# Optimization experiments

Measured on AMD Instinct MI355X. Metric: run time of the kernel, lower is better.

Reference implementation:

```python
import jax, jax.numpy as jnp
from jax import lax
import numpy as np

EPS = 1e-5


def ref_points(Hk, Wk):
    # torch linspace(0.5, Hk-0.5, Hk)/Hk * 2 - 1, stacked (y, x)
    ys = (jnp.linspace(0.5, Hk - 0.5, Hk) / Hk) * 2.0 - 1.0
    xs = (jnp.linspace(0.5, Wk - 0.5, Wk) / Wk) * 2.0 - 1.0
    yy, xx = jnp.meshgrid(ys, xs, indexing='ij')
    return jnp.stack([yy, xx], axis=-1)  # (Hk, Wk, 2) in (y, x) order


def grid_sample(img, grid):
    # Bilinear, align_corners=True, zeros padding (torch F.grid_sample defaults).
    # img: (N, C, Hi, Wi); grid: (N, Hg, Wg, 2) with (x, y) in [-1, 1].
    N, C, Hi, Wi = img.shape
    Hg, Wg = grid.shape[1], grid.shape[2]
    gx = (grid[..., 0] + 1.0) * 0.5 * (Wi - 1)
    gy = (grid[..., 1] + 1.0) * 0.5 * (Hi - 1)
    x0 = jnp.floor(gx)
    y0 = jnp.floor(gy)
    wx1 = gx - x0
    wy1 = gy - y0
    imgf = img.reshape(N, C, Hi * Wi)

    def corner(ix, iy, w):
        valid = (ix >= 0) & (ix < Wi) & (iy >= 0) & (iy < Hi)
        idx = (jnp.clip(iy, 0, Hi - 1).astype(jnp.int32) * Wi
               + jnp.clip(ix, 0, Wi - 1).astype(jnp.int32)).reshape(N, -1)
        vals = jax.vmap(lambda im, f: im[:, f])(imgf, idx)  # (N, C, Hg*Wg)
        return vals * (w * valid).reshape(N, 1, -1)

    out = (corner(x0, y0, (1 - wx1) * (1 - wy1))
           + corner(x0 + 1, y0, wx1 * (1 - wy1))
           + corner(x0, y0 + 1, (1 - wx1) * wy1)
           + corner(x0 + 1, y0 + 1, wx1 * wy1))
    return out.reshape(N, C, Hg, Wg)


def setup_inputs() -> dict:
    key = jax.random.key(0)
    ks = jax.random.split(key, 8)
    B, C, H, W = 8, 128, 64, 64
    gc, nH = 64, 4
    return {
        'x': jax.random.normal(ks[0], (B, C, H, W), jnp.float32),
        'w_dw': jax.random.normal(ks[1], (gc, 1, 5, 5), jnp.float32) * 0.1,
        'ln_w': jnp.ones((gc,), jnp.float32),
        'w_off': jax.random.normal(ks[2], (3, gc), jnp.float32) * 0.1,
        'wq': jax.random.normal(ks[3], (C, C), jnp.float32) * 0.05,
        'wk': jax.random.normal(ks[4], (C, C), jnp.float32) * 0.05,
        'wv': jax.random.normal(ks[5], (C, C), jnp.float32) * 0.05,
        'wo': jax.random.normal(ks[6], (C, C), jnp.float32) * 0.05,
        'rpe': jax.random.normal(ks[7], (nH, 2 * H - 1, 2 * W - 1), jnp.float32) * 0.01,
    }


def reference(x, w_dw, ln_w, w_off, wq, wk, wv, wo, rpe):
    B, C, H, W = x.shape
    G, nH = 2, 4
    gc = C // G           # group channels
    dh = C // nH          # head channels
    gh = nH // G          # heads per group
    scale = dh ** -0.5
    orf = 1.0             # offset_range_factor

    conv1x1 = lambda t, w: jnp.einsum('oi,bihw->bohw', w, t)

    q = conv1x1(x, wq)                                    # (B, C, H, W)
    q_off = q.reshape(B * G, gc, H, W)

    # conv_offset: depthwise 5x5 stride 4 pad 2 -> BiasFree LN (over C) -> GELU -> 1x1 to 3
    off = lax.conv_general_dilated(q_off, w_dw, (4, 4), ((2, 2), (2, 2)),
                                   dimension_numbers=('NCHW', 'OIHW', 'NCHW'),
                                   feature_group_count=gc)  # (B*G, gc, Hk, Wk)
    var = jnp.var(off, axis=1, keepdims=True)
    off = off / jnp.sqrt(var + EPS) * ln_w.reshape(1, -1, 1, 1)
    off = jax.nn.gelu(off, approximate=False)
    off = jnp.einsum('oi,bihw->bohw', w_off, off)          # (B*G, 3, Hk, Wk)

    Hk, Wk = off.shape[2], off.shape[3]
    n = Hk * Wk

    # channel 0 = y offset, channel 1 = x offset, channel 2 = modulation
    offset = jnp.stack([jnp.tanh(off[:, 0]) * (orf / Hk),
                        jnp.tanh(off[:, 1]) * (orf / Wk)], axis=-1)  # (B*G, Hk, Wk, 2) (y,x)
    dm = jax.nn.sigmoid(off[:, 2])[:, None]                # (B*G, 1, Hk, Wk)

    pos = offset + ref_points(Hk, Wk)[None]                # (B*G, Hk, Wk, 2) (y,x)

    xs = grid_sample(x.reshape(B * G, gc, H, W), pos[..., ::-1])  # grid in (x,y)
    xs = (xs * dm).reshape(B, C, 1, n)

    k = conv1x1(xs, wk).reshape(B * nH, dh, n)
    v = conv1x1(xs, wv).reshape(B * nH, dh, n)
    qf = q.reshape(B * nH, dh, H * W)

    attn = jnp.einsum('bcm,bcn->bmn', qf, k) * scale       # (B*nH, H*W, n)

    # relative-position bias sampled at continuous displacements
    rpe_b = jnp.broadcast_to(rpe[None], (B, nH, 2 * H - 1, 2 * W - 1)
                             ).reshape(B * G, gh, 2 * H - 1, 2 * W - 1)
    qg = ref_points(H, W).reshape(H * W, 2)                # (H*W, 2)
    disp = (qg[None, :, None, :] - pos.reshape(B * G, 1, n, 2)) * 0.5  # (B*G, H*W, n, 2)
    bias = grid_sample(rpe_b, disp[..., ::-1]).reshape(B * nH, H * W, n)

    attn = jax.nn.softmax(attn + bias, axis=2)
    out = jnp.einsum('bmn,bcn->bcm', attn, v).reshape(B, C, H, W)
    return conv1x1(out, wo)
```

## Files before the change

kernel.cpp:

```cpp
#include <hip/hip_runtime.h>
#include <hip/hip_bf16.h>
#include <math.h>

#define HW 4096
#define NCH 128

typedef __attribute__((ext_vector_type(8))) short short8;
typedef __attribute__((ext_vector_type(4))) float f32x4;

__device__ __forceinline__ short f2bf(float f) {
  union { __hip_bfloat16 h; short s; } u;
  u.h = __float2bfloat16(f);
  return u.s;
}
__device__ __forceinline__ float bf2f(short s) {
  union { unsigned u; float f; } u;
  u.u = ((unsigned)(unsigned short)s) << 16;
  return u.f;
}

__global__ __launch_bounds__(256) void xq_kernel(
    const float* __restrict__ x, const float* __restrict__ wq,
    short* __restrict__ xT, float* __restrict__ qT) {
  __shared__ float s[128][65];
  int tid = threadIdx.x;
  int b = blockIdx.y;
  int m0 = blockIdx.x * 64;
  {
    int ml = tid & 63, ch = tid >> 6;
#pragma unroll
    for (int i = 0; i < 32; ++i) {
      int c = i * 4 + ch;
      s[c][ml] = x[((size_t)(b * NCH + c)) * HW + m0 + ml];
    }
  }
  __syncthreads();
  {
    int c = tid & 127, mh = tid >> 7;
#pragma unroll
    for (int i = 0; i < 32; ++i) {
      int m = i * 2 + mh;
      xT[((size_t)(b * HW + m0 + m)) * NCH + c] = f2bf(s[c][m]);
    }
  }
  int w = tid >> 6, lane = tid & 63, l15 = lane & 15, qd = lane >> 4;
  int mrow = w * 16 + l15;
  f32x4 acc[8];
#pragma unroll
  for (int ot = 0; ot < 8; ++ot) acc[ot] = (f32x4){0.f, 0.f, 0.f, 0.f};
#pragma unroll
  for (int kc = 0; kc < 4; ++kc) {
    short8 ah, al;
#pragma unroll
    for (int j = 0; j < 8; ++j) {
      float v = s[kc * 32 + qd * 8 + j][mrow];
      short hi = f2bf(v);
      ah[j] = hi;
      al[j] = f2bf(v - bf2f(hi));
    }
#pragma unroll
    for (int ot = 0; ot < 8; ++ot) {
      const float* wr = wq + (size_t)(ot * 16 + l15) * NCH + kc * 32 + qd * 8;
      f32x4 w0 = *(const f32x4*)wr;
      f32x4 w1 = *(const f32x4*)(wr + 4);
      short8 bh, bl;
#pragma unroll
      for (int j = 0; j < 4; ++j) {
        short h0 = f2bf(w0[j]);
        bh[j] = h0;
        bl[j] = f2bf(w0[j] - bf2f(h0));
        short h1 = f2bf(w1[j]);
        bh[4 + j] = h1;
        bl[4 + j] = f2bf(w1[j] - bf2f(h1));
      }
      acc[ot] = __builtin_amdgcn_mfma_f32_16x16x32_bf16(ah, bh, acc[ot], 0, 0, 0);
      acc[ot] = __builtin_amdgcn_mfma_f32_16x16x32_bf16(al, bh, acc[ot], 0, 0, 0);
      acc[ot] = __builtin_amdgcn_mfma_f32_16x16x32_bf16(ah, bl, acc[ot], 0, 0, 0);
    }
  }
#pragma unroll
  for (int ot = 0; ot < 8; ++ot)
#pragma unroll
    for (int r = 0; r < 4; ++r)
      qT[((size_t)(b * HW + m0 + w * 16 + qd * 4 + r)) * NCH + ot * 16 + l15] =
          acc[ot][r];
}

__device__ __forceinline__ float wsum64(float v) {
#pragma unroll
  for (int o = 32; o > 0; o >>= 1) v += __shfl_xor(v, o);
  return v;
}

__global__ __launch_bounds__(256) void conv_offset_kernel(
    const float* __restrict__ qT, const float* __restrict__ w_dw,
    const float* __restrict__ ln_w, const float* __restrict__ w_off,
    const float* __restrict__ wk, const float* __restrict__ wv,
    const float* __restrict__ wo, const float* __restrict__ rpe,
    float* __restrict__ pos, float* __restrict__ dm,
    short* __restrict__ wk_bf, short* __restrict__ wv_bf,
    short* __restrict__ wo_bf, unsigned* __restrict__ tab) {
  int tid = threadIdx.x;
  if (blockIdx.x >= 64) {
    int id = (blockIdx.x - 64) * 16 + blockIdx.y;
    if (id < 64) {
      int i = id * 256 + tid;
      wk_bf[i] = f2bf(wk[i]);
      wv_bf[i] = f2bf(wv[i]);
      wo_bf[i] = f2bf(wo[i]);
    } else {
      int i = (id - 64) * 256 + tid;
      int h = i >> 14, r = i & 16383;
      int row = r >> 7, col = r & 127;
      float lo = 0.f, hi = 0.f;
      if (col < 127) {
        if (row >= 1) lo = rpe[h * 16129 + (row - 1) * 127 + col];
        if (row < 127) hi = rpe[h * 16129 + row * 127 + col];
      }
      union { unsigned u; _Float16 h2[2]; } pk;
      pk.h2[0] = (_Float16)lo;
      pk.h2[1] = (_Float16)hi;
      tab[i] = pk.u;
    }
    return;
  }
  int c = tid & 63;
  int p = blockIdx.x * 4 + (tid >> 6);
  int bg = blockIdx.y;
  int py = p >> 4, px = p & 15;
  const float* qp = qT + (size_t)(bg >> 1) * HW * NCH + (bg & 1) * 64 + c;
  const float* wd = w_dw + c * 25;
  float acc = 0.f;
#pragma unroll
  for (int ky = 0; ky < 5; ++ky) {
    int iy = 4 * py + ky - 2;
    if (iy < 0 || iy >= 64) continue;
#pragma unroll
    for (int kx = 0; kx < 5; ++kx) {
      int ix = 4 * px + kx - 2;
      if (ix < 0 || ix >= 64) continue;
      acc += wd[ky * 5 + kx] * qp[(size_t)(iy * 64 + ix) * NCH];
    }
  }
  float mean = wsum64(acc) * (1.f / 64.f);
  float msq = wsum64(acc * acc) * (1.f / 64.f);
  float var = msq - mean * mean;
  float g = acc * rsqrtf(var + 1e-5f) * ln_w[c];
  g = 0.5f * g * (1.f + erff(g * 0.70710678118654752f));
  float o0 = wsum64(w_off[c] * g);
  float o1 = wsum64(w_off[64 + c] * g);
  float o2 = wsum64(w_off[128 + c] * g);
  if (c == 0) {
    int idx = bg * 256 + p;
    pos[idx * 2] = tanhf(o0) * (1.f / 16.f) + ((py + 0.5f) * (1.f / 8.f) - 1.f);
    pos[idx * 2 + 1] = tanhf(o1) * (1.f / 16.f) + ((px + 0.5f) * (1.f / 8.f) - 1.f);
    dm[idx] = 1.f / (1.f + expf(-o2));
  }
}

__global__ __launch_bounds__(256) void sample_xs_kernel(
    const short* __restrict__ xT, const float* __restrict__ pos,
    const float* __restrict__ dm, short* __restrict__ xsT) {
  int tid = threadIdx.x;
  int c = tid & 63;
  int p = blockIdx.y * 4 + (tid >> 6);
  int bg = blockIdx.x;
  int b = bg >> 1, ch0 = (bg & 1) * 64;
  int idx = bg * 256 + p;
  float posy = pos[idx * 2], posx = pos[idx * 2 + 1];
  float dmv = dm[idx];
  float gx = (posx + 1.f) * 31.5f;
  float gy = (posy + 1.f) * 31.5f;
  float x0f = floorf(gx), y0f = floorf(gy);
  int ix = (int)x0f, iy = (int)y0f;
  float fx = gx - x0f, fy = gy - y0f;
  float w00 = (1.f - fx) * (1.f - fy), w10 = fx * (1.f - fy);
  float w01 = (1.f - fx) * fy, w11 = fx * fy;
  bool vx0 = (ix >= 0 && ix < 64), vx1 = (ix + 1 >= 0 && ix + 1 < 64);
  bool vy0 = (iy >= 0 && iy < 64), vy1 = (iy + 1 >= 0 && iy + 1 < 64);
  if (!(vx0 && vy0)) w00 = 0.f;
  if (!(vx1 && vy0)) w10 = 0.f;
  if (!(vx0 && vy1)) w01 = 0.f;
  if (!(vx1 && vy1)) w11 = 0.f;
  int x0c = min(max(ix, 0), 63), x1c = min(max(ix + 1, 0), 63);
  int y0c = min(max(iy, 0), 63), y1c = min(max(iy + 1, 0), 63);
  size_t rb = (size_t)b * HW * NCH + ch0 + c;
  float v = w00 * bf2f(xT[rb + (size_t)(y0c * 64 + x0c) * NCH]) +
            w10 * bf2f(xT[rb + (size_t)(y0c * 64 + x1c) * NCH]) +
            w01 * bf2f(xT[rb + (size_t)(y1c * 64 + x0c) * NCH]) +
            w11 * bf2f(xT[rb + (size_t)(y1c * 64 + x1c) * NCH]);
  xsT[((size_t)(b * 256 + p)) * NCH + ch0 + c] = f2bf(v * dmv);
}

__global__ __launch_bounds__(256) void kv_mfma_kernel(
    const short* __restrict__ xsT, const short* __restrict__ wk_bf,
    const short* __restrict__ wv_bf, short* __restrict__ kbf,
    short* __restrict__ vbf) {
  int tid = threadIdx.x;
  int w = tid >> 6, lane = tid & 63, l15 = lane & 15, qd = lane >> 4;
  int bh = blockIdx.x, b = bh >> 2;
  int n0 = blockIdx.y * 64 + w * 16;
  f32x4 acc[2];
  acc[0] = (f32x4){0.f, 0.f, 0.f, 0.f};
  acc[1] = (f32x4){0.f, 0.f, 0.f, 0.f};

  size_t xrow = ((size_t)(b * 256 + n0 + l15)) * NCH + qd * 8;
  if (blockIdx.z == 0) {
#pragma unroll
    for (int kc = 0; kc < 4; ++kc) {
      short8 a = *(const short8*)&xsT[xrow + kc * 32];
#pragma unroll
      for (int ot = 0; ot < 2; ++ot) {
        short8 bb = *(const short8*)&wk_bf[(size_t)((bh & 3) * 32 + ot * 16 + l15) * NCH + kc * 32 + qd * 8];
        acc[ot] = __builtin_amdgcn_mfma_f32_16x16x32_bf16(a, bb, acc[ot], 0, 0, 0);
      }
    }
#pragma unroll
    for (int ot = 0; ot < 2; ++ot)
#pragma unroll
      for (int r = 0; r < 4; ++r)
        kbf[((size_t)(bh * 256 + n0 + qd * 4 + r)) * 32 + ot * 16 + l15] =
            f2bf(acc[ot][r]);
  } else {
#pragma unroll
    for (int kc = 0; kc < 4; ++kc) {
      short8 bb = *(const short8*)&xsT[xrow + kc * 32];
#pragma unroll
      for (int ot = 0; ot < 2; ++ot) {
        short8 a = *(const short8*)&wv_bf[(size_t)((bh & 3) * 32 + ot * 16 + l15) * NCH + kc * 32 + qd * 8];
        acc[ot] = __builtin_amdgcn_mfma_f32_16x16x32_bf16(a, bb, acc[ot], 0, 0, 0);
      }
    }
#pragma unroll
    for (int ot = 0; ot < 2; ++ot)
#pragma unroll
      for (int r = 0; r < 4; ++r)
        vbf[((size_t)(bh * 32 + ot * 16 + qd * 4 + r)) * 256 + n0 + l15] =
            f2bf(acc[ot][r]);
  }
}

#define PROW 264
#define TROWS 72

__global__ __launch_bounds__(256) void attn_kernel(
    const float* __restrict__ qT, const short* __restrict__ kbf,
    const short* __restrict__ vbf, const float* __restrict__ pos,
    const unsigned* __restrict__ tabg, short* __restrict__ outT) {
  __shared__ __align__(16) unsigned s_tab[TROWS * 128];
  __shared__ __align__(16) float s_pos[512];
  short* s_p = (short*)s_tab;

  int tid = threadIdx.x;
  int wv = tid >> 6;
  int lane = tid & 63;
  int l15 = lane & 15;
  int qd = lane >> 4;
  int bh = blockIdx.y;
  int b = bh >> 2, h = bh & 3;
  int bg = b * 2 + (h >> 1);
  int m0 = blockIdx.x * 64 + wv * 16;

  float ry = ((float)blockIdx.x + 0.5f) * (1.f / 32.f) - 1.f;
  float gy0 = 63.f + ry * 31.5f;
  int row0 = min(max((int)floorf(gy0) - 34, 0), 128 - TROWS);

  {
    const uint4* src = (const uint4*)(tabg + (size_t)h * 16384 + row0 * 128);
    uint4* dst = (uint4*)s_tab;
#pragma unroll
    for (int i = 0; i < 9; ++i) dst[i * 256 + tid] = src[i * 256 + tid];
    const float* posg = pos + (size_t)bg * 512;
    s_pos[tid] = posg[tid];
    s_pos[256 + tid] = posg[256 + tid];
  }

  short8 qfrag;
  {
    const float* qg = qT + ((size_t)(b * HW + m0 + l15)) * NCH + h * 32 + qd * 8;
    f32x4 a0 = *(const f32x4*)qg;
    f32x4 a1 = *(const f32x4*)(qg + 4);
#pragma unroll
    for (int j = 0; j < 4; ++j) {
      qfrag[j] = f2bf(a0[j]);
      qfrag[4 + j] = f2bf(a1[j]);
    }
  }

  f32x4 acc[16];
  {
    const short* kb = kbf + ((size_t)bh * 256 + l15) * 32 + qd * 8;
#pragma unroll
    for (int t = 0; t < 16; ++t) {
      short8 kf = *(const short8*)(kb + t * 16 * 32);
      acc[t] = __builtin_amdgcn_mfma_f32_16x16x32_bf16(
          kf, qfrag, (f32x4){0.f, 0.f, 0.f, 0.f}, 0, 0, 0);
    }
  }
  __syncthreads();

  int m = m0 + l15;
  float gx0 = ((((float)(m & 63) + 0.5f) * (1.f / 32.f) - 1.f) * 0.5f + 1.f) * 63.f;
  float gyb = gy0 - (float)row0 + 1.f;
  float mx = -1e30f;
#pragma unroll
  for (int t = 0; t < 16; ++t) {
    const f32x4* pp4 = (const f32x4*)&s_pos[(t * 16 + qd * 4) * 2];
    f32x4 pA = pp4[0];
    f32x4 pB = pp4[1];
    float py[4] = {pA[0], pA[2], pB[0], pB[2]};
    float px[4] = {pA[1], pA[3], pB[1], pB[3]};
#pragma unroll
    for (int r = 0; r < 4; ++r) {
      float gy = gyb - py[r] * 31.5f;
      float gx = gx0 - px[r] * 31.5f;
      float y0f = floorf(gy), x0f = floorf(gx);
      float fy = gy - y0f, fx = gx - x0f;
      int row = (int)y0f << 7;
      int xl = (int)x0f;
      unsigned left = s_tab[row + (xl & 127)];
      unsigned right = s_tab[row + xl + 1];
      union { unsigned u; _Float16 h2[2]; } L, R;
      L.u = left;
      R.u = right;
      float t00 = (float)L.h2[0], t01 = (float)L.h2[1];
      float t10 = (float)R.h2[0], t11 = (float)R.h2[1];
      float r0 = t00 + fx * (t10 - t00);
      float r1 = t01 + fx * (t11 - t01);
      float bias = r0 + fy * (r1 - r0);
      float s = fmaf(acc[t][r], 0.17677669529663688f, bias);
      acc[t][r] = s;
      mx = fmaxf(mx, s);
    }
  }
  mx = fmaxf(mx, __shfl_xor(mx, 16));
  float M = fmaxf(mx, __shfl_xor(mx, 32));

  float sm = 0.f;
#pragma unroll
  for (int t = 0; t < 16; ++t) {
#pragma unroll
    for (int r = 0; r < 4; ++r) {
      float e = __expf(acc[t][r] - M);
      acc[t][r] = e;
      sm += e;
    }
  }
  sm += __shfl_xor(sm, 16);
  sm += __shfl_xor(sm, 32);
  float inv = 1.f / sm;

  __syncthreads();

  {
    short* pw = s_p + wv * 16 * PROW + l15 * PROW;
#pragma unroll
    for (int t = 0; t < 16; ++t) {
      int n = t * 16 + qd * 4;
      short4 pk;
      pk.x = f2bf(acc[t][0]);
      pk.y = f2bf(acc[t][1]);
      pk.z = f2bf(acc[t][2]);
      pk.w = f2bf(acc[t][3]);
      *(short4*)(pw + n) = pk;
    }
  }

  f32x4 o0 = {0.f, 0.f, 0.f, 0.f}, o1 = {0.f, 0.f, 0.f, 0.f};
  {
    const short* vb = vbf + ((size_t)bh * 32 + l15) * 256 + qd * 8;
    const short* pr = s_p + wv * 16 * PROW + l15 * PROW + qd * 8;
#pragma unroll
    for (int ch = 0; ch < 8; ++ch) {
      short8 pf = *(const short8*)(pr + ch * 32);
      short8 v0 = *(const short8*)(vb + ch * 32);
      short8 v1 = *(const short8*)(vb + 16 * 256 + ch * 32);
      o0 = __builtin_amdgcn_mfma_f32_16x16x32_bf16(v0, pf, o0, 0, 0, 0);
      o1 = __builtin_amdgcn_mfma_f32_16x16x32_bf16(v1, pf, o1, 0, 0, 0);
    }
  }
  {
    size_t row = (size_t)(b * HW + m0 + l15) * NCH + h * 32 + qd * 4;
    short4 s0, s1;
    s0.x = f2bf(o0[0] * inv); s0.y = f2bf(o0[1] * inv);
    s0.z = f2bf(o0[2] * inv); s0.w = f2bf(o0[3] * inv);
    s1.x = f2bf(o1[0] * inv); s1.y = f2bf(o1[1] * inv);
    s1.z = f2bf(o1[2] * inv); s1.w = f2bf(o1[3] * inv);
    *(short4*)&outT[row] = s0;
    *(short4*)&outT[row + 16] = s1;
  }
}

__global__ __launch_bounds__(256) void wo_mfma_kernel(
    const short* __restrict__ attnT, const short* __restrict__ wo_bf,
    float* __restrict__ out) {
  int tid = threadIdx.x;
  int wv = tid >> 6;
  int lane = tid & 63;
  int l15 = lane & 15;
  int qd = lane >> 4;
  int b = blockIdx.x >> 6;
  int m0 = (blockIdx.x & 63) * 64 + wv * 16;

  f32x4 acc[8];
#pragma unroll
  for (int ot = 0; ot < 8; ++ot) acc[ot] = (f32x4){0.f, 0.f, 0.f, 0.f};

  const short* arow = attnT + (size_t)(b * HW + m0 + l15) * NCH + qd * 8;
  const short* wrow = wo_bf + (size_t)l15 * NCH + qd * 8;
#pragma unroll
  for (int kc = 0; kc < 4; ++kc) {
    short8 afrag = *(const short8*)(arow + kc * 32);
#pragma unroll
    for (int ot = 0; ot < 8; ++ot) {
      short8 bfrag = *(const short8*)(wrow + (size_t)ot * 16 * NCH + kc * 32);
      acc[ot] = __builtin_amdgcn_mfma_f32_16x16x32_bf16(afrag, bfrag, acc[ot],
                                                        0, 0, 0);
    }
  }
#pragma unroll
  for (int ot = 0; ot < 8; ++ot) {
    float* op = out + ((size_t)b * NCH + ot * 16 + l15) * HW + m0 + qd * 4;
    *(f32x4*)op = acc[ot];
  }
}

extern "C" void kernel_launch(void* const* d_in, const int* in_sizes, int n_in,
                              void* d_out, int out_size, void* d_ws,
                              size_t ws_size, hipStream_t stream) {
  const float* x = (const float*)d_in[0];
  const float* w_dw = (const float*)d_in[1];
  const float* ln_w = (const float*)d_in[2];
  const float* w_off = (const float*)d_in[3];
  const float* wq = (const float*)d_in[4];
  const float* wk = (const float*)d_in[5];
  const float* wv = (const float*)d_in[6];
  const float* wo = (const float*)d_in[7];
  const float* rpe = (const float*)d_in[8];
  float* out = (float*)d_out;

  float* qT = out;
  short* sb = (short*)d_ws;
  short* xT = sb;
  short* outT = sb;
  short* xsT = sb + 4194304;
  short* kbf = sb + 4456448;
  short* vbf = sb + 4718592;
  short* wk_bf = sb + 4980736;
  short* wv_bf = sb + 4997120;
  short* wo_bf = sb + 5013504;
  unsigned* tab = (unsigned*)(sb + 5029888);
  float* pos = (float*)(sb + 5160960);
  float* dm = pos + 8192;

  xq_kernel<<<dim3(64, 8), 256, 0, stream>>>(x, wq, xT, qT);
  conv_offset_kernel<<<dim3(84, 16), 256, 0, stream>>>(
      qT, w_dw, ln_w, w_off, wk, wv, wo, rpe, pos, dm, wk_bf, wv_bf, wo_bf,
      tab);
  sample_xs_kernel<<<dim3(16, 64), 256, 0, stream>>>(xT, pos, dm, xsT);
  kv_mfma_kernel<<<dim3(32, 4, 2), 256, 0, stream>>>(xsT, wk_bf, wv_bf, kbf,
                                                     vbf);
  attn_kernel<<<dim3(64, 32), 256, 0, stream>>>(qT, kbf, vbf, pos, tab, outT);
  wo_mfma_kernel<<<512, 256, 0, stream>>>(outT, wo_bf, out);
}
```

Before: 182.2 us.

## Emit bf16 Q copy, split xq and kv grids finer, split softmax reductions

xq_kernel now handles 32 positions per block with each wave computing 4 output tiles, doubling the grid. It also writes a bf16 copy of Q, so attn_kernel loads a ready short8 fragment instead of converting fp32. kv_mfma_kernel splits the output tiles across twice as many blocks. The softmax max and sum now use four independent accumulators to shorten dependency chains. The cost is an extra bf16 Q write and more small blocks.

```diff
diff --git a/kernel.cpp b/kernel.cpp
--- a/kernel.cpp
+++ b/kernel.cpp
@@ -21,16 +21,16 @@
 
 __global__ __launch_bounds__(256) void xq_kernel(
     const float* __restrict__ x, const float* __restrict__ wq,
-    short* __restrict__ xT, float* __restrict__ qT) {
-  __shared__ float s[128][65];
+    short* __restrict__ xT, float* __restrict__ qT, short* __restrict__ qbf) {
+  __shared__ float s[128][33];
   int tid = threadIdx.x;
   int b = blockIdx.y;
-  int m0 = blockIdx.x * 64;
-  {
-    int ml = tid & 63, ch = tid >> 6;
-#pragma unroll
-    for (int i = 0; i < 32; ++i) {
-      int c = i * 4 + ch;
+  int m0 = blockIdx.x * 32;
+  {
+    int ml = tid & 31, c0 = tid >> 5;
+#pragma unroll
+    for (int i = 0; i < 16; ++i) {
+      int c = i * 8 + c0;
       s[c][ml] = x[((size_t)(b * NCH + c)) * HW + m0 + ml];
     }
   }
@@ -38,16 +38,17 @@
   {
     int c = tid & 127, mh = tid >> 7;
 #pragma unroll
-    for (int i = 0; i < 32; ++i) {
+    for (int i = 0; i < 16; ++i) {
       int m = i * 2 + mh;
       xT[((size_t)(b * HW + m0 + m)) * NCH + c] = f2bf(s[c][m]);
     }
   }
   int w = tid >> 6, lane = tid & 63, l15 = lane & 15, qd = lane >> 4;
-  int mrow = w * 16 + l15;
-  f32x4 acc[8];
-#pragma unroll
-  for (int ot = 0; ot < 8; ++ot) acc[ot] = (f32x4){0.f, 0.f, 0.f, 0.f};
+  int mt = w & 1, og = w >> 1;
+  int mrow = mt * 16 + l15;
+  f32x4 acc[4];
+#pragma unroll
+  for (int oi = 0; oi < 4; ++oi) acc[oi] = (f32x4){0.f, 0.f, 0.f, 0.f};
 #pragma unroll
   for (int kc = 0; kc < 4; ++kc) {
     short8 ah, al;
@@ -59,8 +60,9 @@
       al[j] = f2bf(v - bf2f(hi));
     }
 #pragma unroll
-    for (int ot = 0; ot < 8; ++ot) {
-      const float* wr = wq + (size_t)(ot * 16 + l15) * NCH + kc * 32 + qd * 8;
+    for (int oi = 0; oi < 4; ++oi) {
+      const float* wr =
+          wq + (size_t)((og * 4 + oi) * 16 + l15) * NCH + kc * 32 + qd * 8;
       f32x4 w0 = *(const f32x4*)wr;
       f32x4 w1 = *(const f32x4*)(wr + 4);
       short8 bh, bl;
@@ -73,17 +75,20 @@
         bh[4 + j] = h1;
         bl[4 + j] = f2bf(w1[j] - bf2f(h1));
       }
-      acc[ot] = __builtin_amdgcn_mfma_f32_16x16x32_bf16(ah, bh, acc[ot], 0, 0, 0);
-      acc[ot] = __builtin_amdgcn_mfma_f32_16x16x32_bf16(al, bh, acc[ot], 0, 0, 0);
-      acc[ot] = __builtin_amdgcn_mfma_f32_16x16x32_bf16(ah, bl, acc[ot], 0, 0, 0);
-    }
-  }
-#pragma unroll
-  for (int ot = 0; ot < 8; ++ot)
-#pragma unroll
-    for (int r = 0; r < 4; ++r)
-      qT[((size_t)(b * HW + m0 + w * 16 + qd * 4 + r)) * NCH + ot * 16 + l15] =
-          acc[ot][r];
+      acc[oi] = __builtin_amdgcn_mfma_f32_16x16x32_bf16(ah, bh, acc[oi], 0, 0, 0);
+      acc[oi] = __builtin_amdgcn_mfma_f32_16x16x32_bf16(al, bh, acc[oi], 0, 0, 0);
+      acc[oi] = __builtin_amdgcn_mfma_f32_16x16x32_bf16(ah, bl, acc[oi], 0, 0, 0);
+    }
+  }
+#pragma unroll
+  for (int oi = 0; oi < 4; ++oi)
+#pragma unroll
+    for (int r = 0; r < 4; ++r) {
+      size_t idx = ((size_t)(b * HW + m0 + mt * 16 + qd * 4 + r)) * NCH +
+                   og * 64 + oi * 16 + l15;
+      qT[idx] = acc[oi][r];
+      qbf[idx] = f2bf(acc[oi][r]);
+    }
 }
 
 __device__ __forceinline__ float wsum64(float v) {
@@ -200,43 +205,33 @@
   int w = tid >> 6, lane = tid & 63, l15 = lane & 15, qd = lane >> 4;
   int bh = blockIdx.x, b = bh >> 2;
   int n0 = blockIdx.y * 64 + w * 16;
-  f32x4 acc[2];
-  acc[0] = (f32x4){0.f, 0.f, 0.f, 0.f};
-  acc[1] = (f32x4){0.f, 0.f, 0.f, 0.f};
+  int ot = blockIdx.z & 1;
+  f32x4 acc = (f32x4){0.f, 0.f, 0.f, 0.f};
 
   size_t xrow = ((size_t)(b * 256 + n0 + l15)) * NCH + qd * 8;
-  if (blockIdx.z == 0) {
+  size_t wrow = (size_t)((bh & 3) * 32 + ot * 16 + l15) * NCH + qd * 8;
+  if ((blockIdx.z & 2) == 0) {
 #pragma unroll
     for (int kc = 0; kc < 4; ++kc) {
       short8 a = *(const short8*)&xsT[xrow + kc * 32];
-#pragma unroll
-      for (int ot = 0; ot < 2; ++ot) {
-        short8 bb = *(const short8*)&wk_bf[(size_t)((bh & 3) * 32 + ot * 16 + l15) * NCH + kc * 32 + qd * 8];
-        acc[ot] = __builtin_amdgcn_mfma_f32_16x16x32_bf16(a, bb, acc[ot], 0, 0, 0);
-      }
-    }
-#pragma unroll
-    for (int ot = 0; ot < 2; ++ot)
-#pragma unroll
-      for (int r = 0; r < 4; ++r)
-        kbf[((size_t)(bh * 256 + n0 + qd * 4 + r)) * 32 + ot * 16 + l15] =
-            f2bf(acc[ot][r]);
+      short8 bb = *(const short8*)&wk_bf[wrow + kc * 32];
+      acc = __builtin_amdgcn_mfma_f32_16x16x32_bf16(a, bb, acc, 0, 0, 0);
+    }
+#pragma unroll
+    for (int r = 0; r < 4; ++r)
+      kbf[((size_t)(bh * 256 + n0 + qd * 4 + r)) * 32 + ot * 16 + l15] =
+          f2bf(acc[r]);
   } else {
 #pragma unroll
     for (int kc = 0; kc < 4; ++kc) {
       short8 bb = *(const short8*)&xsT[xrow + kc * 32];
-#pragma unroll
-      for (int ot = 0; ot < 2; ++ot) {
-        short8 a = *(const short8*)&wv_bf[(size_t)((bh & 3) * 32 + ot * 16 + l15) * NCH + kc * 32 + qd * 8];
-        acc[ot] = __builtin_amdgcn_mfma_f32_16x16x32_bf16(a, bb, acc[ot], 0, 0, 0);
-      }
-    }
-#pragma unroll
-    for (int ot = 0; ot < 2; ++ot)
-#pragma unroll
-      for (int r = 0; r < 4; ++r)
-        vbf[((size_t)(bh * 32 + ot * 16 + qd * 4 + r)) * 256 + n0 + l15] =
-            f2bf(acc[ot][r]);
+      short8 a = *(const short8*)&wv_bf[wrow + kc * 32];
+      acc = __builtin_amdgcn_mfma_f32_16x16x32_bf16(a, bb, acc, 0, 0, 0);
+    }
+#pragma unroll
+    for (int r = 0; r < 4; ++r)
+      vbf[((size_t)(bh * 32 + ot * 16 + qd * 4 + r)) * 256 + n0 + l15] =
+          f2bf(acc[r]);
   }
 }
 
@@ -244,7 +239,7 @@
 #define TROWS 72
 
 __global__ __launch_bounds__(256) void attn_kernel(
-    const float* __restrict__ qT, const short* __restrict__ kbf,
+    const short* __restrict__ qbf, const short* __restrict__ kbf,
     const short* __restrict__ vbf, const float* __restrict__ pos,
     const unsigned* __restrict__ tabg, short* __restrict__ outT) {
   __shared__ __align__(16) unsigned s_tab[TROWS * 128];
@@ -275,17 +270,8 @@
     s_pos[256 + tid] = posg[256 + tid];
   }
 
-  short8 qfrag;
-  {
-    const float* qg = qT + ((size_t)(b * HW + m0 + l15)) * NCH + h * 32 + qd * 8;
-    f32x4 a0 = *(const f32x4*)qg;
-    f32x4 a1 = *(const f32x4*)(qg + 4);
-#pragma unroll
-    for (int j = 0; j < 4; ++j) {
-      qfrag[j] = f2bf(a0[j]);
-      qfrag[4 + j] = f2bf(a1[j]);
-    }
-  }
+  short8 qfrag =
+      *(const short8*)&qbf[((size_t)(b * HW + m0 + l15)) * NCH + h * 32 + qd * 8];
 
   f32x4 acc[16];
   {
@@ -302,7 +288,7 @@
   int m = m0 + l15;
   float gx0 = ((((float)(m & 63) + 0.5f) * (1.f / 32.f) - 1.f) * 0.5f + 1.f) * 63.f;
   float gyb = gy0 - (float)row0 + 1.f;
-  float mx = -1e30f;
+  float mxA[4] = {-1e30f, -1e30f, -1e30f, -1e30f};
 #pragma unroll
   for (int t = 0; t < 16; ++t) {
     const f32x4* pp4 = (const f32x4*)&s_pos[(t * 16 + qd * 4) * 2];
@@ -330,22 +316,24 @@
       float bias = r0 + fy * (r1 - r0);
       float s = fmaf(acc[t][r], 0.17677669529663688f, bias);
       acc[t][r] = s;
-      mx = fmaxf(mx, s);
-    }
-  }
+      mxA[r] = fmaxf(mxA[r], s);
+    }
+  }
+  float mx = fmaxf(fmaxf(mxA[0], mxA[1]), fmaxf(mxA[2], mxA[3]));
   mx = fmaxf(mx, __shfl_xor(mx, 16));
   float M = fmaxf(mx, __shfl_xor(mx, 32));
 
-  float sm = 0.f;
+  float smA[4] = {0.f, 0.f, 0.f, 0.f};
 #pragma unroll
   for (int t = 0; t < 16; ++t) {
 #pragma unroll
     for (int r = 0; r < 4; ++r) {
       float e = __expf(acc[t][r] - M);
       acc[t][r] = e;
-      sm += e;
-    }
-  }
+      smA[r] += e;
+    }
+  }
+  float sm = (smA[0] + smA[1]) + (smA[2] + smA[3]);
   sm += __shfl_xor(sm, 16);
   sm += __shfl_xor(sm, 32);
   float inv = 1.f / sm;
@@ -452,14 +440,15 @@
   unsigned* tab = (unsigned*)(sb + 5029888);
   float* pos = (float*)(sb + 5160960);
   float* dm = pos + 8192;
-
-  xq_kernel<<<dim3(64, 8), 256, 0, stream>>>(x, wq, xT, qT);
+  short* qbf = sb + 5185536;
+
+  xq_kernel<<<dim3(128, 8), 256, 0, stream>>>(x, wq, xT, qT, qbf);
   conv_offset_kernel<<<dim3(84, 16), 256, 0, stream>>>(
       qT, w_dw, ln_w, w_off, wk, wv, wo, rpe, pos, dm, wk_bf, wv_bf, wo_bf,
       tab);
   sample_xs_kernel<<<dim3(16, 64), 256, 0, stream>>>(xT, pos, dm, xsT);
-  kv_mfma_kernel<<<dim3(32, 4, 2), 256, 0, stream>>>(xsT, wk_bf, wv_bf, kbf,
+  kv_mfma_kernel<<<dim3(32, 4, 4), 256, 0, stream>>>(xsT, wk_bf, wv_bf, kbf,
                                                      vbf);
-  attn_kernel<<<dim3(64, 32), 256, 0, stream>>>(qT, kbf, vbf, pos, tab, outT);
+  attn_kernel<<<dim3(64, 32), 256, 0, stream>>>(qbf, kbf, vbf, pos, tab, outT);
   wo_mfma_kernel<<<512, 256, 0, stream>>>(outT, wo_bf, out);
 }
```

After: 184.2 us. About the same (+1.1%).
